# Kernel optimization log

Measured on AMD Instinct MI355X. Metric: run time of the kernel, lower is better.

Reference implementation:

```python
import jax, jax.numpy as jnp
import numpy as np

OUTPUT_SIZE = 7
STRIDES = (4, 8, 16, 32)
IMG = 1024.0


def setup_inputs() -> dict:
    key = jax.random.key(0)
    ks = jax.random.split(key, 7)
    B, C, N = 2, 256, 1000
    p2 = jax.random.normal(ks[0], (B, 256, 256, C), jnp.float32)
    p3 = jax.random.normal(ks[1], (B, 128, 128, C), jnp.float32)
    p4 = jax.random.normal(ks[2], (B, 64, 64, C), jnp.float32)
    p5 = jax.random.normal(ks[3], (B, 32, 32, C), jnp.float32)
    # box sizes log-uniform in [16, 800] px so all pyramid levels get RoIs
    wh = jnp.exp(jax.random.uniform(ks[4], (N, 2), minval=jnp.log(16.0), maxval=jnp.log(800.0)))
    cxy = jax.random.uniform(ks[5], (N, 2), minval=0.0, maxval=IMG)
    x1y1 = jnp.clip(cxy - wh / 2.0, 0.0, IMG - 1.0)
    x2y2 = jnp.clip(cxy + wh / 2.0, x1y1 + 1.0, IMG - 1.0)
    rois = jnp.concatenate([x1y1, x2y2], axis=1)  # [N,4] = [x1,y1,x2,y2]
    batch_indices = jax.random.randint(ks[6], (N,), 0, B, dtype=jnp.int32)
    return {"p2": p2, "p3": p3, "p4": p4, "p5": p5, "rois": rois, "batch_indices": batch_indices}


def _crop_and_resize(fm, boxes, box_idx, crop):
    """tf.image.crop_and_resize (bilinear, extrapolation_value=0).
    fm: [B,H,W,C]; boxes: [N,4] normalized [y1,x1,y2,x2]; box_idx: [N] int.
    Returns [N, crop, crop, C]."""
    H, W = fm.shape[1], fm.shape[2]
    y1, x1, y2, x2 = boxes[:, 0], boxes[:, 1], boxes[:, 2], boxes[:, 3]
    g = jnp.arange(crop, dtype=fm.dtype) / (crop - 1)  # crop > 1
    in_y = (y1[:, None] + (y2 - y1)[:, None] * g) * (H - 1)  # [N,crop]
    in_x = (x1[:, None] + (x2 - x1)[:, None] * g) * (W - 1)  # [N,crop]
    valid_y = (in_y >= 0) & (in_y <= H - 1)
    valid_x = (in_x >= 0) & (in_x <= W - 1)
    y0 = jnp.floor(in_y); x0 = jnp.floor(in_x)
    ly = in_y - y0; lx = in_x - x0
    y0i = jnp.clip(y0, 0, H - 1).astype(jnp.int32)
    y1i = jnp.clip(jnp.ceil(in_y), 0, H - 1).astype(jnp.int32)
    x0i = jnp.clip(x0, 0, W - 1).astype(jnp.int32)
    x1i = jnp.clip(jnp.ceil(in_x), 0, W - 1).astype(jnp.int32)
    b = box_idx[:, None, None]
    tl = fm[b, y0i[:, :, None], x0i[:, None, :]]  # [N,crop,crop,C]
    tr = fm[b, y0i[:, :, None], x1i[:, None, :]]
    bl = fm[b, y1i[:, :, None], x0i[:, None, :]]
    br = fm[b, y1i[:, :, None], x1i[:, None, :]]
    lxe = lx[:, None, :, None]
    top = tl + (tr - tl) * lxe
    bot = bl + (br - bl) * lxe
    out = top + (bot - top) * ly[:, :, None, None]
    mask = (valid_y[:, :, None] & valid_x[:, None, :])[..., None]
    return jnp.where(mask, out, jnp.zeros((), fm.dtype))


def reference(p2, p3, p4, p5, rois, batch_indices):
    fms = (p2, p3, p4, p5)
    w = rois[:, 2] - rois[:, 0]
    h = rois[:, 3] - rois[:, 1]
    levels = jnp.log(jnp.sqrt(h * w) / 224.0) / jnp.log(2.0) + 4.0
    levels = jnp.clip(jnp.round(levels).astype(jnp.int32), 2, 5)  # [N]
    N = rois.shape[0]
    C = p2.shape[-1]
    c = OUTPUT_SIZE
    out = jnp.zeros((N, c, c, C), p2.dtype)
    for i, stride in enumerate(STRIDES):
        fm = fms[i]
        H, W = fm.shape[1], fm.shape[2]
        bx = rois / float(stride)
        # normalized [y1, x1, y2, x2]
        boxes = jnp.stack([bx[:, 1] / H, bx[:, 0] / W, bx[:, 3] / H, bx[:, 2] / W], axis=1)
        feats = _crop_and_resize(fm, boxes, batch_indices, c)
        mask = (levels == i + 2)[:, None, None, None]
        out = jnp.where(mask, feats, out)
    # boolean-mask + concat + argsort-restore in the original is an identity
    # reordering: result i comes from roi i's assigned level; batch indices
    # are restored to the original order.
    return out, batch_indices
```

## Files before the change

kernel.cpp:

```cpp
#include <hip/hip_runtime.h>
#include <math.h>

#define NCH  256
#define CROP 7

__device__ __forceinline__ float lerpf(float a, float b, float t) {
    return a + (b - a) * t;
}

__global__ __launch_bounds__(256) void roialign_fpn_kernel(
    const float* __restrict__ p2, const float* __restrict__ p3,
    const float* __restrict__ p4, const float* __restrict__ p5,
    const float* __restrict__ rois, const int* __restrict__ bidx,
    float* __restrict__ out)
{
    const int tid = threadIdx.x;
    const int cv  = tid & 63;
    const int pl  = tid >> 6;
    const int pix = blockIdx.x * 4 + pl;
    const int n   = blockIdx.y;
    if (pix >= CROP * CROP) return;
    const int jy = pix / CROP;
    const int jx = pix - jy * CROP;

    const float rx1 = rois[4*n+0];
    const float ry1 = rois[4*n+1];
    const float rx2 = rois[4*n+2];
    const float ry2 = rois[4*n+3];
    const float w = rx2 - rx1;
    const float h = ry2 - ry1;

    const float lvlf = logf(sqrtf(h * w) / 224.0f) / logf(2.0f) + 4.0f;
    int lvl = (int)rintf(lvlf);
    lvl = lvl < 2 ? 2 : (lvl > 5 ? 5 : lvl);
    const int i = lvl - 2;

    const int H = 256 >> i;
    const float* fm = (i == 0) ? p2 : (i == 1) ? p3 : (i == 2) ? p4 : p5;
    const float inv = 1.0f / (float)((4 << i) * H);
    const float Hm1 = (float)(H - 1);

    const float gy = (float)jy / 6.0f;
    const float gx = (float)jx / 6.0f;
    const float ny1 = ry1 * inv, ny2 = ry2 * inv;
    const float nx1 = rx1 * inv, nx2 = rx2 * inv;
    const float in_y = (ny1 + (ny2 - ny1) * gy) * Hm1;
    const float in_x = (nx1 + (nx2 - nx1) * gx) * Hm1;

    const bool valid = (in_y >= 0.0f) && (in_y <= Hm1) &&
                       (in_x >= 0.0f) && (in_x <= Hm1);

    const float y0f = floorf(in_y);
    const float x0f = floorf(in_x);
    const float ly = in_y - y0f;
    const float lx = in_x - x0f;
    const int y0 = (int)fminf(fmaxf(y0f,          0.0f), Hm1);
    const int y1 = (int)fminf(fmaxf(ceilf(in_y),  0.0f), Hm1);
    const int x0 = (int)fminf(fmaxf(x0f,          0.0f), Hm1);
    const int x1 = (int)fminf(fmaxf(ceilf(in_x),  0.0f), Hm1);

    const int b = bidx[n];
    const size_t row0 = ((size_t)b * H + y0) * (size_t)H;
    const size_t row1 = ((size_t)b * H + y1) * (size_t)H;
    const int c = cv * 4;

    const float4 tl = *(const float4*)(fm + (row0 + x0) * NCH + c);
    const float4 tr = *(const float4*)(fm + (row0 + x1) * NCH + c);
    const float4 bl = *(const float4*)(fm + (row1 + x0) * NCH + c);
    const float4 br = *(const float4*)(fm + (row1 + x1) * NCH + c);

    float4 r;
    r.x = lerpf(lerpf(tl.x, tr.x, lx), lerpf(bl.x, br.x, lx), ly);
    r.y = lerpf(lerpf(tl.y, tr.y, lx), lerpf(bl.y, br.y, lx), ly);
    r.z = lerpf(lerpf(tl.z, tr.z, lx), lerpf(bl.z, br.z, lx), ly);
    r.w = lerpf(lerpf(tl.w, tr.w, lx), lerpf(bl.w, br.w, lx), ly);
    if (!valid) { r.x = 0.0f; r.y = 0.0f; r.z = 0.0f; r.w = 0.0f; }

    *(float4*)(out + ((size_t)n * (CROP * CROP) + pix) * NCH + c) = r;
}

__global__ void bidx_copy_kernel(const int* __restrict__ bidx,
                                 float* __restrict__ out_tail, int N)
{
    const int g = blockIdx.x * blockDim.x + threadIdx.x;
    if (g < N) out_tail[g] = (float)bidx[g];
}

extern "C" void kernel_launch(void* const* d_in, const int* in_sizes, int n_in,
                              void* d_out, int out_size, void* d_ws, size_t ws_size,
                              hipStream_t stream) {
    const float* p2   = (const float*)d_in[0];
    const float* p3   = (const float*)d_in[1];
    const float* p4   = (const float*)d_in[2];
    const float* p5   = (const float*)d_in[3];
    const float* rois = (const float*)d_in[4];
    const int*   bidx = (const int*)d_in[5];
    float* out = (float*)d_out;

    const int N = in_sizes[5];

    dim3 grid((CROP * CROP + 3) / 4, N);
    roialign_fpn_kernel<<<grid, 256, 0, stream>>>(p2, p3, p4, p5, rois, bidx, out);

    float* tail = out + (size_t)N * (CROP * CROP * NCH);
    bidx_copy_kernel<<<(N + 255) / 256, 256, 0, stream>>>(bidx, tail, N);
}
```

Baseline: 224.8 us.

## Use one block per RoI, fuse batch-index copy, use nontemporal stores

Each RoI now gets a single block of 256 threads, which loops over all 49 crop pixels four at a time instead of launching 13 blocks per RoI. The per-RoI level and box setup is computed once per block. The separate batch-index copy kernel is folded into the main kernel, which removes one launch. Output writes use nontemporal stores so the write-once output does not pollute the cache, at the cost of fewer blocks and less parallelism across the grid.

Result: no change. 226.7 us (+0.9%).

```diff
diff --git a/kernel.cpp b/kernel.cpp
--- a/kernel.cpp
+++ b/kernel.cpp
@@ -3,6 +3,8 @@
 
 #define NCH  256
 #define CROP 7
+
+typedef float v4f __attribute__((ext_vector_type(4)));
 
 __device__ __forceinline__ float lerpf(float a, float b, float t) {
     return a + (b - a) * t;
@@ -12,16 +14,12 @@
     const float* __restrict__ p2, const float* __restrict__ p3,
     const float* __restrict__ p4, const float* __restrict__ p5,
     const float* __restrict__ rois, const int* __restrict__ bidx,
-    float* __restrict__ out)
+    float* __restrict__ out, int N)
 {
     const int tid = threadIdx.x;
     const int cv  = tid & 63;
     const int pl  = tid >> 6;
-    const int pix = blockIdx.x * 4 + pl;
-    const int n   = blockIdx.y;
-    if (pix >= CROP * CROP) return;
-    const int jy = pix / CROP;
-    const int jx = pix - jy * CROP;
+    const int n   = blockIdx.x;
 
     const float rx1 = rois[4*n+0];
     const float ry1 = rois[4*n+1];
@@ -40,50 +38,56 @@
     const float inv = 1.0f / (float)((4 << i) * H);
     const float Hm1 = (float)(H - 1);
 
-    const float gy = (float)jy / 6.0f;
-    const float gx = (float)jx / 6.0f;
     const float ny1 = ry1 * inv, ny2 = ry2 * inv;
     const float nx1 = rx1 * inv, nx2 = rx2 * inv;
-    const float in_y = (ny1 + (ny2 - ny1) * gy) * Hm1;
-    const float in_x = (nx1 + (nx2 - nx1) * gx) * Hm1;
-
-    const bool valid = (in_y >= 0.0f) && (in_y <= Hm1) &&
-                       (in_x >= 0.0f) && (in_x <= Hm1);
-
-    const float y0f = floorf(in_y);
-    const float x0f = floorf(in_x);
-    const float ly = in_y - y0f;
-    const float lx = in_x - x0f;
-    const int y0 = (int)fminf(fmaxf(y0f,          0.0f), Hm1);
-    const int y1 = (int)fminf(fmaxf(ceilf(in_y),  0.0f), Hm1);
-    const int x0 = (int)fminf(fmaxf(x0f,          0.0f), Hm1);
-    const int x1 = (int)fminf(fmaxf(ceilf(in_x),  0.0f), Hm1);
 
     const int b = bidx[n];
-    const size_t row0 = ((size_t)b * H + y0) * (size_t)H;
-    const size_t row1 = ((size_t)b * H + y1) * (size_t)H;
+    const size_t bbase = (size_t)b * H;
     const int c = cv * 4;
+    float* outn = out + (size_t)n * (CROP * CROP * NCH) + c;
 
-    const float4 tl = *(const float4*)(fm + (row0 + x0) * NCH + c);
-    const float4 tr = *(const float4*)(fm + (row0 + x1) * NCH + c);
-    const float4 bl = *(const float4*)(fm + (row1 + x0) * NCH + c);
-    const float4 br = *(const float4*)(fm + (row1 + x1) * NCH + c);
+    if (tid == 0)
+        out[(size_t)N * (CROP * CROP * NCH) + n] = (float)b;
 
-    float4 r;
-    r.x = lerpf(lerpf(tl.x, tr.x, lx), lerpf(bl.x, br.x, lx), ly);
-    r.y = lerpf(lerpf(tl.y, tr.y, lx), lerpf(bl.y, br.y, lx), ly);
-    r.z = lerpf(lerpf(tl.z, tr.z, lx), lerpf(bl.z, br.z, lx), ly);
-    r.w = lerpf(lerpf(tl.w, tr.w, lx), lerpf(bl.w, br.w, lx), ly);
-    if (!valid) { r.x = 0.0f; r.y = 0.0f; r.z = 0.0f; r.w = 0.0f; }
+    #pragma unroll 2
+    for (int pix = pl; pix < CROP * CROP; pix += 4) {
+        const int jy = pix / CROP;
+        const int jx = pix - jy * CROP;
 
-    *(float4*)(out + ((size_t)n * (CROP * CROP) + pix) * NCH + c) = r;
-}
+        const float gy = (float)jy / 6.0f;
+        const float gx = (float)jx / 6.0f;
+        const float in_y = (ny1 + (ny2 - ny1) * gy) * Hm1;
+        const float in_x = (nx1 + (nx2 - nx1) * gx) * Hm1;
 
-__global__ void bidx_copy_kernel(const int* __restrict__ bidx,
-                                 float* __restrict__ out_tail, int N)
-{
-    const int g = blockIdx.x * blockDim.x + threadIdx.x;
-    if (g < N) out_tail[g] = (float)bidx[g];
+        const bool valid = (in_y >= 0.0f) && (in_y <= Hm1) &&
+                           (in_x >= 0.0f) && (in_x <= Hm1);
+
+        const float y0f = floorf(in_y);
+        const float x0f = floorf(in_x);
+        const float ly = in_y - y0f;
+        const float lx = in_x - x0f;
+        const int y0 = (int)fminf(fmaxf(y0f,          0.0f), Hm1);
+        const int y1 = (int)fminf(fmaxf(ceilf(in_y),  0.0f), Hm1);
+        const int x0 = (int)fminf(fmaxf(x0f,          0.0f), Hm1);
+        const int x1 = (int)fminf(fmaxf(ceilf(in_x),  0.0f), Hm1);
+
+        const size_t row0 = (bbase + y0) * (size_t)H;
+        const size_t row1 = (bbase + y1) * (size_t)H;
+
+        const v4f tl = *(const v4f*)(fm + (row0 + x0) * NCH + c);
+        const v4f tr = *(const v4f*)(fm + (row0 + x1) * NCH + c);
+        const v4f bl = *(const v4f*)(fm + (row1 + x0) * NCH + c);
+        const v4f br = *(const v4f*)(fm + (row1 + x1) * NCH + c);
+
+        v4f r;
+        r.x = lerpf(lerpf(tl.x, tr.x, lx), lerpf(bl.x, br.x, lx), ly);
+        r.y = lerpf(lerpf(tl.y, tr.y, lx), lerpf(bl.y, br.y, lx), ly);
+        r.z = lerpf(lerpf(tl.z, tr.z, lx), lerpf(bl.z, br.z, lx), ly);
+        r.w = lerpf(lerpf(tl.w, tr.w, lx), lerpf(bl.w, br.w, lx), ly);
+        if (!valid) { r.x = 0.0f; r.y = 0.0f; r.z = 0.0f; r.w = 0.0f; }
+
+        __builtin_nontemporal_store(r, (v4f*)(outn + (size_t)pix * NCH));
+    }
 }
 
 extern "C" void kernel_launch(void* const* d_in, const int* in_sizes, int n_in,
@@ -99,9 +103,6 @@
 
     const int N = in_sizes[5];
 
-    dim3 grid((CROP * CROP + 3) / 4, N);
-    roialign_fpn_kernel<<<grid, 256, 0, stream>>>(p2, p3, p4, p5, rois, bidx, out);
-
-    float* tail = out + (size_t)N * (CROP * CROP * NCH);
-    bidx_copy_kernel<<<(N + 255) / 256, 256, 0, stream>>>(bidx, tail, N);
+    roialign_fpn_kernel<<<dim3(N), 256, 0, stream>>>(p2, p3, p4, p5, rois, bidx,
+                                                     out, N);
 }
```
